# Optimization experiments

Hardware: AMD Instinct MI355X
Metric: run time of the kernel (lower is better)

## Reference

```python
import jax, jax.numpy as jnp
import numpy as np

NEG_INF = -1e9


def setup_inputs() -> dict:
    key = jax.random.key(0)
    ks = jax.random.split(key, 6)
    B, S, ENC, DEC = 32, 2048, 1024, 1024
    decoder_hidden = jax.random.normal(ks[0], (B, DEC), dtype=jnp.float32)
    encoder_outputs = jax.random.normal(ks[1], (B, S, ENC), dtype=jnp.float32)
    mask = jax.random.randint(ks[2], (B, S), 0, 2, dtype=jnp.int32)
    # nn.Linear-style weights, scaled ~ 1/sqrt(fan_in)
    W_h = jax.random.normal(ks[3], (DEC, ENC), dtype=jnp.float32) / np.sqrt(ENC)
    W_s = jax.random.normal(ks[4], (DEC, DEC), dtype=jnp.float32) / np.sqrt(DEC)
    v = jax.random.normal(ks[5], (DEC,), dtype=jnp.float32) / np.sqrt(DEC)
    return {
        "decoder_hidden": decoder_hidden,
        "encoder_outputs": encoder_outputs,
        "mask": mask,
        "W_h": W_h,
        "W_s": W_s,
        "v": v,
    }


def reference(decoder_hidden, encoder_outputs, mask, W_h, W_s, v):
    # dec: [B, D] -> [B, 1, D]
    dec = jnp.einsum("bd,ed->be", decoder_hidden, W_s)[:, None, :]
    # enc: [B, S, E] -> [B, S, D]
    enc = jnp.einsum("bse,de->bsd", encoder_outputs, W_h)
    # energy: [B, S] via rank-1 projection with v
    energy = jnp.einsum("bsd,d->bs", jnp.tanh(enc + dec), v)
    energy = jnp.where(mask == 0, NEG_INF, energy)
    attn_weights = jax.nn.softmax(energy, axis=1)  # [B, S]
    # context: [B, E]
    context = jnp.einsum("bs,bse->be", attn_weights, encoder_outputs)
    return (context, attn_weights)
```

## Files before the change

### kernel.cpp

```cpp
#include <hip/hip_runtime.h>
#include <stdint.h>
#include <math.h>

typedef __attribute__((ext_vector_type(8))) short short8;
typedef __attribute__((ext_vector_type(4))) float f32x4;

#define S_LEN 2048
#define NBATCH 32
#define KDIM 1024
#define NEG_INF_F (-1e9f)

#define BM 256
#define BN 256

__device__ __forceinline__ uint32_t pack_bf16(float f0, float f1) {
    union { float f; uint32_t u; } a, b; a.f = f0; b.f = f1;
    return ((a.u + 0x8000u) >> 16) | ((b.u + 0x8000u) & 0xFFFF0000u);
}

__device__ __forceinline__ void gload_lds16(const unsigned short* g, unsigned short* l) {
    __builtin_amdgcn_global_load_lds(
        (const __attribute__((address_space(1))) void*)g,
        (__attribute__((address_space(3))) void*)l, 16, 0, 0);
}

__device__ __forceinline__ float fast_tanh(float x) {
    float e = __expf(2.0f * x);
    return 1.0f - 2.0f * __builtin_amdgcn_rcpf(e + 1.0f);
}

__global__ __launch_bounds__(256) void dec_kernel(
    const float* __restrict__ dh, const float* __restrict__ Ws,
    float* __restrict__ dec)
{
    __shared__ float wrow[1024];
    int e = blockIdx.x;
    int t = threadIdx.x;
    #pragma unroll
    for (int i = t; i < 1024; i += 256) wrow[i] = Ws[(size_t)e * 1024 + i];
    __syncthreads();
    int b = t >> 3, part = t & 7;
    const float* dhp = dh + (size_t)b * 1024 + part * 128;
    const float* wp  = wrow + part * 128;
    float s = 0.f;
    #pragma unroll 8
    for (int i = 0; i < 128; ++i) s += dhp[i] * wp[i];
    s += __shfl_xor(s, 1);
    s += __shfl_xor(s, 2);
    s += __shfl_xor(s, 4);
    if (part == 0) dec[(size_t)b * 1024 + e] = s;
}

__global__ __launch_bounds__(256) void convert_frag(
    const float* __restrict__ src, unsigned short* __restrict__ hi, int lg_nmsub)
{
    int gid = blockIdx.x * 4 + (threadIdx.x >> 6);
    int lane = threadIdx.x & 63;
    int ms = gid & ((1 << lg_nmsub) - 1);
    int ks = gid >> lg_nmsub;
    const float* p = src + (size_t)(ms * 16 + (lane & 15)) * 1024
                         + ks * 32 + (lane >> 4) * 8;
    f32x4 a = *(const f32x4*)p;
    f32x4 b = *(const f32x4*)(p + 4);
    union { uint32_t d[4]; short8 v; } o;
    o.d[0] = pack_bf16(a.x, a.y); o.d[1] = pack_bf16(a.z, a.w);
    o.d[2] = pack_bf16(b.x, b.y); o.d[3] = pack_bf16(b.z, b.w);
    *(short8*)(hi + (size_t)gid * 512 + lane * 8) = o.v;
}

__global__ __launch_bounds__(512, 2) void energy_gemm_v6(
    const unsigned short* __restrict__ Ahi,
    const unsigned short* __restrict__ Bhi,
    const float* __restrict__ dec, const float* __restrict__ v,
    float* __restrict__ energy)
{
    __shared__ unsigned short lds[32768];

    int bid = blockIdx.x;
    int lid = (bid & 7) * 128 + (bid >> 3);
    int mblk = lid >> 2, nblk = lid & 3;
    int m0 = mblk * BM, n0 = nblk * BN;
    int b = m0 >> 11;

    int t = threadIdx.x, wid = t >> 6, lane = t & 63;
    int wm = wid >> 2, wn = wid & 3;
    int kg = lane >> 4, lr = lane & 15;

    f32x4 acc[8][4] = {};

    #pragma unroll
    for (int i = 0; i < 4; ++i) {
        int c = wid * 4 + i;
        const unsigned short* g = (c < 16)
            ? Ahi + ((size_t)mblk * 16 + c) * 512
            : Bhi + ((size_t)nblk * 16 + (c - 16)) * 512;
        gload_lds16(g + lane * 8, &lds[c * 512]);
    }
    asm volatile("s_waitcnt vmcnt(0)" ::: "memory");
    __builtin_amdgcn_s_barrier();

    for (int ks = 0; ks < 32; ++ks) {
        unsigned short* bufA = &lds[(ks & 1) * 16384];
        unsigned short* bufB = bufA + 8192;

        if (ks < 31) {
            unsigned short* nbuf = &lds[((ks + 1) & 1) * 16384];
            #pragma unroll
            for (int i = 0; i < 4; ++i) {
                int c = wid * 4 + i;
                const unsigned short* g = (c < 16)
                    ? Ahi + ((size_t)(ks + 1) * 4096 + mblk * 16 + c) * 512
                    : Bhi + ((size_t)(ks + 1) * 64 + nblk * 16 + (c - 16)) * 512;
                gload_lds16(g + lane * 8, &nbuf[c * 512]);
            }
        }

        short8 bf[4];
        #pragma unroll
        for (int ni = 0; ni < 4; ++ni)
            bf[ni] = *(const short8*)&bufB[(wn * 4 + ni) * 512 + lane * 8];
        #pragma unroll
        for (int mi = 0; mi < 8; ++mi) {
            short8 af = *(const short8*)&bufA[(wm * 8 + mi) * 512 + lane * 8];
            #pragma unroll
            for (int ni = 0; ni < 4; ++ni)
                acc[mi][ni] = __builtin_amdgcn_mfma_f32_16x16x32_bf16(af, bf[ni], acc[mi][ni], 0, 0, 0);
        }

        asm volatile("s_waitcnt vmcnt(0)" ::: "memory");
        __builtin_amdgcn_s_barrier();
    }

    float vv[4], dd[4];
    #pragma unroll
    for (int ni = 0; ni < 4; ++ni) {
        int d = n0 + wn * 64 + ni * 16 + lr;
        vv[ni] = v[d];
        dd[ni] = dec[(size_t)b * 1024 + d];
    }
    #pragma unroll
    for (int mi = 0; mi < 8; ++mi) {
        #pragma unroll
        for (int r = 0; r < 4; ++r) {
            float local = 0.f;
            #pragma unroll
            for (int ni = 0; ni < 4; ++ni)
                local += fast_tanh(acc[mi][ni][r] + dd[ni]) * vv[ni];
            local += __shfl_xor(local, 1);
            local += __shfl_xor(local, 2);
            local += __shfl_xor(local, 4);
            local += __shfl_xor(local, 8);
            if (lr == 0) {
                int m = m0 + wm * 128 + mi * 16 + kg * 4 + r;
                atomicAdd(&energy[m], local);
            }
        }
    }
}

__global__ __launch_bounds__(256) void softmax_kernel(
    const float* __restrict__ energy, const int* __restrict__ mask,
    float* __restrict__ attn)
{
    int b = blockIdx.x;
    int t = threadIdx.x;
    int wid = t >> 6, lane = t & 63;
    __shared__ float wmax[4], wsum[4];

    float vals[8];
    float mx = -INFINITY;
    #pragma unroll
    for (int j = 0; j < 8; ++j) {
        int s = t + j * 256;
        float e = energy[(size_t)b * S_LEN + s];
        if (mask[(size_t)b * S_LEN + s] == 0) e = NEG_INF_F;
        vals[j] = e;
        mx = fmaxf(mx, e);
    }
    #pragma unroll
    for (int m = 1; m < 64; m <<= 1) mx = fmaxf(mx, __shfl_xor(mx, m));
    if (lane == 0) wmax[wid] = mx;
    __syncthreads();
    mx = fmaxf(fmaxf(wmax[0], wmax[1]), fmaxf(wmax[2], wmax[3]));

    float sum = 0.f;
    #pragma unroll
    for (int j = 0; j < 8; ++j) { vals[j] = expf(vals[j] - mx); sum += vals[j]; }
    #pragma unroll
    for (int m = 1; m < 64; m <<= 1) sum += __shfl_xor(sum, m);
    if (lane == 0) wsum[wid] = sum;
    __syncthreads();
    sum = wsum[0] + wsum[1] + wsum[2] + wsum[3];
    float inv = 1.f / sum;
    #pragma unroll
    for (int j = 0; j < 8; ++j)
        attn[(size_t)b * S_LEN + t + j * 256] = vals[j] * inv;
}

__global__ __launch_bounds__(256) void context_kernel(
    const float* __restrict__ attn, const float* __restrict__ x,
    float* __restrict__ ctx)
{
    int ec = blockIdx.x, b = blockIdx.y, sc = blockIdx.z;
    int e = ec * 256 + threadIdx.x;
    const float* xp = x + ((size_t)b * S_LEN + sc * 128) * KDIM + e;
    const float* ap = attn + (size_t)b * S_LEN + sc * 128;
    float acc = 0.f;
    #pragma unroll 4
    for (int s = 0; s < 128; ++s) acc += ap[s] * xp[(size_t)s * KDIM];
    atomicAdd(&ctx[(size_t)b * KDIM + e], acc);
}

extern "C" void kernel_launch(void* const* d_in, const int* in_sizes, int n_in,
                              void* d_out, int out_size, void* d_ws, size_t ws_size,
                              hipStream_t stream) {
    const float* dh   = (const float*)d_in[0];
    const float* x    = (const float*)d_in[1];
    const int*   mask = (const int*)d_in[2];
    const float* Wh   = (const float*)d_in[3];
    const float* Ws   = (const float*)d_in[4];
    const float* v    = (const float*)d_in[5];

    float* ctx  = (float*)d_out;
    float* attn = (float*)d_out + 32 * 1024;

    unsigned short* Ahi = (unsigned short*)d_ws;
    unsigned short* Bhi = Ahi + 67108864ull;
    float* dec    = (float*)(Bhi + 1048576ull);
    float* energy = dec + 32768;

    hipMemsetAsync(energy, 0, 65536 * sizeof(float), stream);
    hipMemsetAsync(ctx, 0, 32768 * sizeof(float), stream);

    dec_kernel<<<1024, 256, 0, stream>>>(dh, Ws, dec);
    convert_frag<<<512, 256, 0, stream>>>(Wh, Bhi, 6);
    convert_frag<<<32768, 256, 0, stream>>>(x, Ahi, 12);
    energy_gemm_v6<<<1024, 512, 0, stream>>>(Ahi, Bhi, dec, v, energy);
    softmax_kernel<<<NBATCH, 256, 0, stream>>>(energy, mask, attn);
    context_kernel<<<dim3(4, NBATCH, 16), 256, 0, stream>>>(attn, x, ctx);
}
```

Baseline: 317.3 us.

## Triple-buffer GEMM LDS pipeline with split loads, priority hints, and reordered A conversion

The energy GEMM now uses three LDS stages instead of two and prefetches two k-steps ahead. Each step's A reads and MFMA work is split into four phases, with global-to-LDS staging spread across them and s_setprio raised around the MFMA bursts, so memory traffic overlaps compute and barriers no longer stall on a full vmcnt(0). The A conversion kernel changes its block-to-tile mapping so each workgroup walks along K for one row tile, making its reads more contiguous while keeping the same fragment output layout. This raises LDS use per block and adds many more barriers, which could limit occupancy or add sync overhead.

```diff
diff --git a/kernel.cpp b/kernel.cpp
--- a/kernel.cpp
+++ b/kernel.cpp
@@ -51,13 +51,12 @@
     if (part == 0) dec[(size_t)b * 1024 + e] = s;
 }
 
-__global__ __launch_bounds__(256) void convert_frag(
-    const float* __restrict__ src, unsigned short* __restrict__ hi, int lg_nmsub)
+__global__ __launch_bounds__(256) void convert_frag_B(
+    const float* __restrict__ src, unsigned short* __restrict__ out)
 {
     int gid = blockIdx.x * 4 + (threadIdx.x >> 6);
     int lane = threadIdx.x & 63;
-    int ms = gid & ((1 << lg_nmsub) - 1);
-    int ks = gid >> lg_nmsub;
+    int ms = gid & 63, ks = gid >> 6;
     const float* p = src + (size_t)(ms * 16 + (lane & 15)) * 1024
                          + ks * 32 + (lane >> 4) * 8;
     f32x4 a = *(const f32x4*)p;
@@ -65,16 +64,32 @@
     union { uint32_t d[4]; short8 v; } o;
     o.d[0] = pack_bf16(a.x, a.y); o.d[1] = pack_bf16(a.z, a.w);
     o.d[2] = pack_bf16(b.x, b.y); o.d[3] = pack_bf16(b.z, b.w);
-    *(short8*)(hi + (size_t)gid * 512 + lane * 8) = o.v;
-}
-
-__global__ __launch_bounds__(512, 2) void energy_gemm_v6(
+    *(short8*)(out + (size_t)gid * 512 + lane * 8) = o.v;
+}
+
+__global__ __launch_bounds__(256) void convert_frag_A(
+    const float* __restrict__ src, unsigned short* __restrict__ out)
+{
+    int gid = blockIdx.x * 4 + (threadIdx.x >> 6);
+    int lane = threadIdx.x & 63;
+    int ms = gid >> 5, ks = gid & 31;
+    const float* p = src + (size_t)(ms * 16 + (lane & 15)) * 1024
+                         + ks * 32 + (lane >> 4) * 8;
+    f32x4 a = *(const f32x4*)p;
+    f32x4 b = *(const f32x4*)(p + 4);
+    union { uint32_t d[4]; short8 v; } o;
+    o.d[0] = pack_bf16(a.x, a.y); o.d[1] = pack_bf16(a.z, a.w);
+    o.d[2] = pack_bf16(b.x, b.y); o.d[3] = pack_bf16(b.z, b.w);
+    *(short8*)(out + ((size_t)ks * 4096 + ms) * 512 + lane * 8) = o.v;
+}
+
+__global__ __launch_bounds__(512, 2) void energy_gemm_v7(
     const unsigned short* __restrict__ Ahi,
     const unsigned short* __restrict__ Bhi,
     const float* __restrict__ dec, const float* __restrict__ v,
     float* __restrict__ energy)
 {
-    __shared__ unsigned short lds[32768];
+    __shared__ unsigned short lds[49152];
 
     int bid = blockIdx.x;
     int lid = (bid & 7) * 128 + (bid >> 3);
@@ -88,47 +103,73 @@
 
     f32x4 acc[8][4] = {};
 
-    #pragma unroll
-    for (int i = 0; i < 4; ++i) {
-        int c = wid * 4 + i;
-        const unsigned short* g = (c < 16)
-            ? Ahi + ((size_t)mblk * 16 + c) * 512
-            : Bhi + ((size_t)nblk * 16 + (c - 16)) * 512;
-        gload_lds16(g + lane * 8, &lds[c * 512]);
-    }
-    asm volatile("s_waitcnt vmcnt(0)" ::: "memory");
-    __builtin_amdgcn_s_barrier();
-
+    auto stage2 = [&](int t2, int sbase, int i0) {
+        #pragma unroll
+        for (int i = i0; i < i0 + 2; ++i) {
+            int c = wid * 4 + i;
+            const unsigned short* g = (c < 16)
+                ? Ahi + ((size_t)t2 * 4096 + mblk * 16 + c) * 512
+                : Bhi + ((size_t)t2 * 64 + nblk * 16 + (c - 16)) * 512;
+            gload_lds16(g + lane * 8, &lds[sbase + c * 512]);
+        }
+    };
+
+#define RD_A(buf, mi) (*(const short8*)&(buf)[(wm * 8 + (mi)) * 512 + lane * 8])
+#define RD_B(buf, ni) (*(const short8*)&(buf)[8192 + (wn * 4 + (ni)) * 512 + lane * 8])
+#define MFMA4(mi, AF) \
+    acc[mi][0] = __builtin_amdgcn_mfma_f32_16x16x32_bf16(AF, bf0, acc[mi][0], 0, 0, 0); \
+    acc[mi][1] = __builtin_amdgcn_mfma_f32_16x16x32_bf16(AF, bf1, acc[mi][1], 0, 0, 0); \
+    acc[mi][2] = __builtin_amdgcn_mfma_f32_16x16x32_bf16(AF, bf2, acc[mi][2], 0, 0, 0); \
+    acc[mi][3] = __builtin_amdgcn_mfma_f32_16x16x32_bf16(AF, bf3, acc[mi][3], 0, 0, 0);
+#define BAR()   __builtin_amdgcn_s_barrier()
+#define LGKM0() asm volatile("s_waitcnt lgkmcnt(0)" ::: "memory")
+#define PRIO1() __builtin_amdgcn_s_setprio(1)
+#define PRIO0() __builtin_amdgcn_s_setprio(0)
+
+    stage2(0, 0, 0);     stage2(0, 0, 2);
+    stage2(1, 16384, 0); stage2(1, 16384, 2);
+    asm volatile("s_waitcnt vmcnt(4)" ::: "memory");
+    BAR();
+
+    int cb = 0;
     for (int ks = 0; ks < 32; ++ks) {
-        unsigned short* bufA = &lds[(ks & 1) * 16384];
-        unsigned short* bufB = bufA + 8192;
-
-        if (ks < 31) {
-            unsigned short* nbuf = &lds[((ks + 1) & 1) * 16384];
-            #pragma unroll
-            for (int i = 0; i < 4; ++i) {
-                int c = wid * 4 + i;
-                const unsigned short* g = (c < 16)
-                    ? Ahi + ((size_t)(ks + 1) * 4096 + mblk * 16 + c) * 512
-                    : Bhi + ((size_t)(ks + 1) * 64 + nblk * 16 + (c - 16)) * 512;
-                gload_lds16(g + lane * 8, &nbuf[c * 512]);
-            }
-        }
-
-        short8 bf[4];
-        #pragma unroll
-        for (int ni = 0; ni < 4; ++ni)
-            bf[ni] = *(const short8*)&bufB[(wn * 4 + ni) * 512 + lane * 8];
-        #pragma unroll
-        for (int mi = 0; mi < 8; ++mi) {
-            short8 af = *(const short8*)&bufA[(wm * 8 + mi) * 512 + lane * 8];
-            #pragma unroll
-            for (int ni = 0; ni < 4; ++ni)
-                acc[mi][ni] = __builtin_amdgcn_mfma_f32_16x16x32_bf16(af, bf[ni], acc[mi][ni], 0, 0, 0);
-        }
-
-        asm volatile("s_waitcnt vmcnt(0)" ::: "memory");
-        __builtin_amdgcn_s_barrier();
+        int sb = cb + 2; if (sb >= 3) sb -= 3;
+        unsigned short* buf = &lds[cb * 16384];
+        const int sbase = sb * 16384;
+        const bool st = (ks < 30);
+
+        short8 bf0 = RD_B(buf, 0), bf1 = RD_B(buf, 1);
+        short8 bf2 = RD_B(buf, 2), bf3 = RD_B(buf, 3);
+        {
+            short8 af0 = RD_A(buf, 0), af1 = RD_A(buf, 1);
+            if (st) stage2(ks + 2, sbase, 0);
+            BAR(); LGKM0(); PRIO1();
+            MFMA4(0, af0); MFMA4(1, af1);
+            PRIO0(); BAR();
+        }
+        {
+            short8 af2 = RD_A(buf, 2), af3 = RD_A(buf, 3);
+            if (st) stage2(ks + 2, sbase, 2);
+            BAR(); LGKM0(); PRIO1();
+            MFMA4(2, af2); MFMA4(3, af3);
+            PRIO0(); BAR();
+        }
+        {
+            short8 af4 = RD_A(buf, 4), af5 = RD_A(buf, 5);
+            BAR(); LGKM0(); PRIO1();
+            MFMA4(4, af4); MFMA4(5, af5);
+            PRIO0(); BAR();
+        }
+        {
+            short8 af6 = RD_A(buf, 6), af7 = RD_A(buf, 7);
+            BAR(); LGKM0(); PRIO1();
+            MFMA4(6, af6); MFMA4(7, af7);
+            PRIO0();
+            if (st) asm volatile("s_waitcnt vmcnt(4)" ::: "memory");
+            else    asm volatile("s_waitcnt vmcnt(0)" ::: "memory");
+            BAR();
+        }
+        cb = cb + 1; if (cb >= 3) cb -= 3;
     }
 
     float vv[4], dd[4];
@@ -233,9 +274,9 @@
     hipMemsetAsync(ctx, 0, 32768 * sizeof(float), stream);
 
     dec_kernel<<<1024, 256, 0, stream>>>(dh, Ws, dec);
-    convert_frag<<<512, 256, 0, stream>>>(Wh, Bhi, 6);
-    convert_frag<<<32768, 256, 0, stream>>>(x, Ahi, 12);
-    energy_gemm_v6<<<1024, 512, 0, stream>>>(Ahi, Bhi, dec, v, energy);
+    convert_frag_B<<<512, 256, 0, stream>>>(Wh, Bhi);
+    convert_frag_A<<<32768, 256, 0, stream>>>(x, Ahi);
+    energy_gemm_v7<<<1024, 512, 0, stream>>>(Ahi, Bhi, dec, v, energy);
     softmax_kernel<<<NBATCH, 256, 0, stream>>>(energy, mask, attn);
     context_kernel<<<dim3(4, NBATCH, 16), 256, 0, stream>>>(attn, x, ctx);
 }
```

Measured after the change: 311.4 us. About the same (-1.9%).

## Fuse fp32-to-bf16 conversion of encoder outputs into the energy GEMM

Applied to the files above, without the earlier changes.

Removes the standalone conversion kernel for the encoder outputs and the bf16 workspace copy. The GEMM now loads fp32 rows of x directly into registers, packs them to bf16 and writes them into the LDS double buffer, while the weight fragments still stream via global-to-LDS loads. This cuts a large write and re-read pass through HBM but makes each M tile read fp32 data once per N block, doubling per-GEMM A-operand bytes and adding VGPR pressure and conversion ALU work inside the main loop.

```diff
diff --git a/kernel.cpp b/kernel.cpp
--- a/kernel.cpp
+++ b/kernel.cpp
@@ -51,13 +51,12 @@
     if (part == 0) dec[(size_t)b * 1024 + e] = s;
 }
 
-__global__ __launch_bounds__(256) void convert_frag(
-    const float* __restrict__ src, unsigned short* __restrict__ hi, int lg_nmsub)
+__global__ __launch_bounds__(256) void convert_frag_B(
+    const float* __restrict__ src, unsigned short* __restrict__ out)
 {
     int gid = blockIdx.x * 4 + (threadIdx.x >> 6);
     int lane = threadIdx.x & 63;
-    int ms = gid & ((1 << lg_nmsub) - 1);
-    int ks = gid >> lg_nmsub;
+    int ms = gid & 63, ks = gid >> 6;
     const float* p = src + (size_t)(ms * 16 + (lane & 15)) * 1024
                          + ks * 32 + (lane >> 4) * 8;
     f32x4 a = *(const f32x4*)p;
@@ -65,11 +64,11 @@
     union { uint32_t d[4]; short8 v; } o;
     o.d[0] = pack_bf16(a.x, a.y); o.d[1] = pack_bf16(a.z, a.w);
     o.d[2] = pack_bf16(b.x, b.y); o.d[3] = pack_bf16(b.z, b.w);
-    *(short8*)(hi + (size_t)gid * 512 + lane * 8) = o.v;
-}
-
-__global__ __launch_bounds__(512, 2) void energy_gemm_v6(
-    const unsigned short* __restrict__ Ahi,
+    *(short8*)(out + (size_t)gid * 512 + lane * 8) = o.v;
+}
+
+__global__ __launch_bounds__(512, 2) void energy_gemm_v8(
+    const float* __restrict__ x,
     const unsigned short* __restrict__ Bhi,
     const float* __restrict__ dec, const float* __restrict__ v,
     float* __restrict__ energy)
@@ -88,31 +87,50 @@
 
     f32x4 acc[8][4] = {};
 
-    #pragma unroll
-    for (int i = 0; i < 4; ++i) {
-        int c = wid * 4 + i;
-        const unsigned short* g = (c < 16)
-            ? Ahi + ((size_t)mblk * 16 + c) * 512
-            : Bhi + ((size_t)nblk * 16 + (c - 16)) * 512;
-        gload_lds16(g + lane * 8, &lds[c * 512]);
-    }
-    asm volatile("s_waitcnt vmcnt(0)" ::: "memory");
+    int arow0 = m0 + (wid * 16) + (lane & 15);
+    const float* apb0 = x + (size_t)arow0 * KDIM + (lane >> 4) * 8;
+    const float* apb1 = apb0 + (size_t)128 * KDIM;
+    int wa0 = wid * 512 + lane * 8;
+    int wa1 = wa0 + 8 * 512;
+
+    auto stageB = [&](int ksb, unsigned short* buf) {
+        #pragma unroll
+        for (int i = 0; i < 2; ++i) {
+            int c = wid * 2 + i;
+            gload_lds16(Bhi + ((size_t)ksb * 64 + nblk * 16 + c) * 512 + lane * 8,
+                        &buf[8192 + c * 512]);
+        }
+    };
+
+    f32x4 a0, a1, a2, a3;
+
+    stageB(0, &lds[0]);
+    a0 = *(const f32x4*)apb0; a1 = *(const f32x4*)(apb0 + 4);
+    a2 = *(const f32x4*)apb1; a3 = *(const f32x4*)(apb1 + 4);
+    {
+        union { uint32_t d[4]; short8 v; } o;
+        o.d[0] = pack_bf16(a0.x, a0.y); o.d[1] = pack_bf16(a0.z, a0.w);
+        o.d[2] = pack_bf16(a1.x, a1.y); o.d[3] = pack_bf16(a1.z, a1.w);
+        *(short8*)&lds[wa0] = o.v;
+        o.d[0] = pack_bf16(a2.x, a2.y); o.d[1] = pack_bf16(a2.z, a2.w);
+        o.d[2] = pack_bf16(a3.x, a3.y); o.d[3] = pack_bf16(a3.z, a3.w);
+        *(short8*)&lds[wa1] = o.v;
+    }
+    asm volatile("s_waitcnt vmcnt(0) lgkmcnt(0)" ::: "memory");
     __builtin_amdgcn_s_barrier();
 
     for (int ks = 0; ks < 32; ++ks) {
         unsigned short* bufA = &lds[(ks & 1) * 16384];
         unsigned short* bufB = bufA + 8192;
-
-        if (ks < 31) {
-            unsigned short* nbuf = &lds[((ks + 1) & 1) * 16384];
-            #pragma unroll
-            for (int i = 0; i < 4; ++i) {
-                int c = wid * 4 + i;
-                const unsigned short* g = (c < 16)
-                    ? Ahi + ((size_t)(ks + 1) * 4096 + mblk * 16 + c) * 512
-                    : Bhi + ((size_t)(ks + 1) * 64 + nblk * 16 + (c - 16)) * 512;
-                gload_lds16(g + lane * 8, &nbuf[c * 512]);
-            }
+        unsigned short* nbuf = &lds[((ks + 1) & 1) * 16384];
+        const bool st = (ks < 31);
+
+        if (st) {
+            const float* p0 = apb0 + (ks + 1) * 32;
+            const float* p1 = apb1 + (ks + 1) * 32;
+            a0 = *(const f32x4*)p0; a1 = *(const f32x4*)(p0 + 4);
+            a2 = *(const f32x4*)p1; a3 = *(const f32x4*)(p1 + 4);
+            stageB(ks + 1, nbuf);
         }
 
         short8 bf[4];
@@ -127,7 +145,17 @@
                 acc[mi][ni] = __builtin_amdgcn_mfma_f32_16x16x32_bf16(af, bf[ni], acc[mi][ni], 0, 0, 0);
         }
 
-        asm volatile("s_waitcnt vmcnt(0)" ::: "memory");
+        if (st) {
+            union { uint32_t d[4]; short8 v; } o;
+            o.d[0] = pack_bf16(a0.x, a0.y); o.d[1] = pack_bf16(a0.z, a0.w);
+            o.d[2] = pack_bf16(a1.x, a1.y); o.d[3] = pack_bf16(a1.z, a1.w);
+            *(short8*)&nbuf[wa0] = o.v;
+            o.d[0] = pack_bf16(a2.x, a2.y); o.d[1] = pack_bf16(a2.z, a2.w);
+            o.d[2] = pack_bf16(a3.x, a3.y); o.d[3] = pack_bf16(a3.z, a3.w);
+            *(short8*)&nbuf[wa1] = o.v;
+        }
+
+        asm volatile("s_waitcnt vmcnt(0) lgkmcnt(0)" ::: "memory");
         __builtin_amdgcn_s_barrier();
     }
 
@@ -224,8 +252,7 @@
     float* ctx  = (float*)d_out;
     float* attn = (float*)d_out + 32 * 1024;
 
-    unsigned short* Ahi = (unsigned short*)d_ws;
-    unsigned short* Bhi = Ahi + 67108864ull;
+    unsigned short* Bhi = (unsigned short*)d_ws;
     float* dec    = (float*)(Bhi + 1048576ull);
     float* energy = dec + 32768;
 
@@ -233,9 +260,8 @@
     hipMemsetAsync(ctx, 0, 32768 * sizeof(float), stream);
 
     dec_kernel<<<1024, 256, 0, stream>>>(dh, Ws, dec);
-    convert_frag<<<512, 256, 0, stream>>>(Wh, Bhi, 6);
-    convert_frag<<<32768, 256, 0, stream>>>(x, Ahi, 12);
-    energy_gemm_v6<<<1024, 512, 0, stream>>>(Ahi, Bhi, dec, v, energy);
+    convert_frag_B<<<512, 256, 0, stream>>>(Wh, Bhi);
+    energy_gemm_v8<<<1024, 512, 0, stream>>>(x, Bhi, dec, v, energy);
     softmax_kernel<<<NBATCH, 256, 0, stream>>>(energy, mask, attn);
     context_kernel<<<dim3(4, NBATCH, 16), 256, 0, stream>>>(attn, x, ctx);
 }
```

After: 357.8 us. +12.8%, slower.

## Double K-step per GEMM stage and reorder A conversion for contiguous reads

Applied to the files above, without the earlier changes.

The energy GEMM now stages two K-slices (64 of K) per barrier iteration, with double-buffered LDS grown to 128KB, which halves the number of barriers and waits. The A conversion kernel now walks ms-major/ks-minor, so consecutive workgroups read contiguous rows of x, while it still writes in the ks-major fragment layout. The larger LDS footprint may cut occupancy below the requested 2 blocks per CU, since 128KB per block could exceed the LDS available on a CU.

```diff
diff --git a/kernel.cpp b/kernel.cpp
--- a/kernel.cpp
+++ b/kernel.cpp
@@ -51,13 +51,12 @@
     if (part == 0) dec[(size_t)b * 1024 + e] = s;
 }
 
-__global__ __launch_bounds__(256) void convert_frag(
-    const float* __restrict__ src, unsigned short* __restrict__ hi, int lg_nmsub)
+__global__ __launch_bounds__(256) void convert_frag_B(
+    const float* __restrict__ src, unsigned short* __restrict__ out)
 {
     int gid = blockIdx.x * 4 + (threadIdx.x >> 6);
     int lane = threadIdx.x & 63;
-    int ms = gid & ((1 << lg_nmsub) - 1);
-    int ks = gid >> lg_nmsub;
+    int ms = gid & 63, ks = gid >> 6;
     const float* p = src + (size_t)(ms * 16 + (lane & 15)) * 1024
                          + ks * 32 + (lane >> 4) * 8;
     f32x4 a = *(const f32x4*)p;
@@ -65,16 +64,32 @@
     union { uint32_t d[4]; short8 v; } o;
     o.d[0] = pack_bf16(a.x, a.y); o.d[1] = pack_bf16(a.z, a.w);
     o.d[2] = pack_bf16(b.x, b.y); o.d[3] = pack_bf16(b.z, b.w);
-    *(short8*)(hi + (size_t)gid * 512 + lane * 8) = o.v;
-}
-
-__global__ __launch_bounds__(512, 2) void energy_gemm_v6(
+    *(short8*)(out + (size_t)gid * 512 + lane * 8) = o.v;
+}
+
+__global__ __launch_bounds__(256) void convert_frag_A(
+    const float* __restrict__ src, unsigned short* __restrict__ out)
+{
+    int gid = blockIdx.x * 4 + (threadIdx.x >> 6);
+    int lane = threadIdx.x & 63;
+    int ms = gid >> 5, ks = gid & 31;
+    const float* p = src + (size_t)(ms * 16 + (lane & 15)) * 1024
+                         + ks * 32 + (lane >> 4) * 8;
+    f32x4 a = *(const f32x4*)p;
+    f32x4 b = *(const f32x4*)(p + 4);
+    union { uint32_t d[4]; short8 v; } o;
+    o.d[0] = pack_bf16(a.x, a.y); o.d[1] = pack_bf16(a.z, a.w);
+    o.d[2] = pack_bf16(b.x, b.y); o.d[3] = pack_bf16(b.z, b.w);
+    *(short8*)(out + ((size_t)ks * 4096 + ms) * 512 + lane * 8) = o.v;
+}
+
+__global__ __launch_bounds__(512, 2) void energy_gemm_v9(
     const unsigned short* __restrict__ Ahi,
     const unsigned short* __restrict__ Bhi,
     const float* __restrict__ dec, const float* __restrict__ v,
     float* __restrict__ energy)
 {
-    __shared__ unsigned short lds[32768];
+    __shared__ unsigned short lds[65536];
 
     int bid = blockIdx.x;
     int lid = (bid & 7) * 128 + (bid >> 3);
@@ -88,43 +103,46 @@
 
     f32x4 acc[8][4] = {};
 
-    #pragma unroll
-    for (int i = 0; i < 4; ++i) {
-        int c = wid * 4 + i;
-        const unsigned short* g = (c < 16)
-            ? Ahi + ((size_t)mblk * 16 + c) * 512
-            : Bhi + ((size_t)nblk * 16 + (c - 16)) * 512;
-        gload_lds16(g + lane * 8, &lds[c * 512]);
-    }
+    auto stage = [&](int t2, unsigned short* buf) {
+        #pragma unroll
+        for (int i = 0; i < 4; ++i) {
+            int c = wid * 4 + i;
+            int ks = 2 * t2 + (c >> 4);
+            gload_lds16(Ahi + ((size_t)ks * 4096 + mblk * 16 + (c & 15)) * 512 + lane * 8,
+                        &buf[c * 512]);
+        }
+        #pragma unroll
+        for (int i = 0; i < 4; ++i) {
+            int c = wid * 4 + i;
+            int ks = 2 * t2 + (c >> 4);
+            gload_lds16(Bhi + ((size_t)ks * 64 + nblk * 16 + (c & 15)) * 512 + lane * 8,
+                        &buf[16384 + c * 512]);
+        }
+    };
+
+    stage(0, &lds[0]);
     asm volatile("s_waitcnt vmcnt(0)" ::: "memory");
     __builtin_amdgcn_s_barrier();
 
-    for (int ks = 0; ks < 32; ++ks) {
-        unsigned short* bufA = &lds[(ks & 1) * 16384];
-        unsigned short* bufB = bufA + 8192;
-
-        if (ks < 31) {
-            unsigned short* nbuf = &lds[((ks + 1) & 1) * 16384];
-            #pragma unroll
-            for (int i = 0; i < 4; ++i) {
-                int c = wid * 4 + i;
-                const unsigned short* g = (c < 16)
-                    ? Ahi + ((size_t)(ks + 1) * 4096 + mblk * 16 + c) * 512
-                    : Bhi + ((size_t)(ks + 1) * 64 + nblk * 16 + (c - 16)) * 512;
-                gload_lds16(g + lane * 8, &nbuf[c * 512]);
-            }
-        }
-
-        short8 bf[4];
-        #pragma unroll
-        for (int ni = 0; ni < 4; ++ni)
-            bf[ni] = *(const short8*)&bufB[(wn * 4 + ni) * 512 + lane * 8];
-        #pragma unroll
-        for (int mi = 0; mi < 8; ++mi) {
-            short8 af = *(const short8*)&bufA[(wm * 8 + mi) * 512 + lane * 8];
+    for (int ts = 0; ts < 16; ++ts) {
+        unsigned short* bufA = &lds[(ts & 1) * 32768];
+        unsigned short* bufB = bufA + 16384;
+
+        if (ts < 15) stage(ts + 1, &lds[((ts + 1) & 1) * 32768]);
+
+        #pragma unroll
+        for (int ksl = 0; ksl < 2; ++ksl) {
+            short8 bf[4];
             #pragma unroll
             for (int ni = 0; ni < 4; ++ni)
-                acc[mi][ni] = __builtin_amdgcn_mfma_f32_16x16x32_bf16(af, bf[ni], acc[mi][ni], 0, 0, 0);
+                bf[ni] = *(const short8*)&bufB[(ksl * 16 + wn * 4 + ni) * 512 + lane * 8];
+            #pragma unroll
+            for (int mi = 0; mi < 8; ++mi) {
+                short8 af = *(const short8*)&bufA[(ksl * 16 + wm * 8 + mi) * 512 + lane * 8];
+                #pragma unroll
+                for (int ni = 0; ni < 4; ++ni)
+                    acc[mi][ni] = __builtin_amdgcn_mfma_f32_16x16x32_bf16(af, bf[ni], acc[mi][ni], 0, 0, 0);
+            }
         }
 
         asm volatile("s_waitcnt vmcnt(0)" ::: "memory");
@@ -233,9 +251,9 @@
     hipMemsetAsync(ctx, 0, 32768 * sizeof(float), stream);
 
     dec_kernel<<<1024, 256, 0, stream>>>(dh, Ws, dec);
-    convert_frag<<<512, 256, 0, stream>>>(Wh, Bhi, 6);
-    convert_frag<<<32768, 256, 0, stream>>>(x, Ahi, 12);
-    energy_gemm_v6<<<1024, 512, 0, stream>>>(Ahi, Bhi, dec, v, energy);
+    convert_frag_B<<<512, 256, 0, stream>>>(Wh, Bhi);
+    convert_frag_A<<<32768, 256, 0, stream>>>(x, Ahi);
+    energy_gemm_v9<<<1024, 512, 0, stream>>>(Ahi, Bhi, dec, v, energy);
     softmax_kernel<<<NBATCH, 256, 0, stream>>>(energy, mask, attn);
     context_kernel<<<dim3(4, NBATCH, 16), 256, 0, stream>>>(attn, x, ctx);
 }
```

Result: faster. 288.7 us (-9.0%).
